# Kernel tuning notes

Hardware: AMD Instinct MI355X
Metric: run time of the kernel (lower is better)

The kernel has to match this reference:

```python
import jax, jax.numpy as jnp
import numpy as np

N = 100000       # nodes
E = 1600000      # edges (avg degree 16)
D = 128          # features_dim = hidden_dim = out_dim
G = 3            # group_num
NUM = 50000      # nodes present in all time groups
ALPHA = 0.2      # LeakyReLU slope
W_SCALE = 0.05


def setup_inputs() -> dict:
    key = jax.random.key(0)
    ks = jax.random.split(key, 8)
    x = jax.random.normal(ks[0], (N, D), jnp.float32)
    edge_index = jax.random.randint(ks[1], (2, E), 0, N, dtype=jnp.int64)
    past = jax.random.normal(ks[2], (G - 1, NUM, D), jnp.float32)
    W1 = jax.random.normal(ks[3], (2 * D, D), jnp.float32) * W_SCALE
    W2 = jax.random.normal(ks[4], (2 * D, D), jnp.float32) * W_SCALE
    W0 = jax.random.normal(ks[5], (D, D), jnp.float32) * W_SCALE
    Wp = jax.random.normal(ks[6], (G - 1, D, D), jnp.float32) * W_SCALE
    W_T = jax.random.normal(ks[7], (2 * D, D), jnp.float32) * W_SCALE
    return {"x": x, "past": past, "W1": W1, "W2": W2, "W0": W0,
            "Wp": Wp, "W_T": W_T, "edge_index": edge_index, "num": NUM}


def reference(x, past, W1, W2, W0, Wp, W_T, edge_index, num):
    src, dst = edge_index[0], edge_index[1]
    n = x.shape[0]
    deg = jax.ops.segment_sum(jnp.ones(src.shape[0], x.dtype), dst, num_segments=n)
    deg = jnp.maximum(deg, 1.0)[:, None]

    def sage_layer(h, W):
        # mean-aggregate neighbors, concat with self, linear + ReLU
        agg = jax.ops.segment_sum(h[src], dst, num_segments=n) / deg
        return jax.nn.relu(jnp.concatenate([h, agg], axis=1) @ W)

    feat = sage_layer(x, W1)      # [N, D]
    feat = sage_layer(feat, W2)   # [N, D]

    # temporal mean aggregation (dropout is identity in eval mode)
    time_feat = (feat[:num] @ W0 + jnp.einsum('knd,kde->ne', past, Wp)) / G
    fused = jnp.concatenate([feat[:num], time_feat], axis=1) @ W_T  # [num, D]
    f = jax.nn.leaky_relu(fused, ALPHA)
    f = f / jnp.maximum(jnp.linalg.norm(f, axis=1, keepdims=True), 1e-12)
    return jnp.concatenate([f, feat[num:]], axis=0)  # [N, D]
```

## Files before the change

kernel.cpp:

```cpp
#include <hip/hip_runtime.h>

#define FD 128
#define CAP 64
#define BSH 8
#define BINSZ 256
#define NBMAX 512
#define BINCAP 4864

typedef __attribute__((ext_vector_type(8))) short bf16x8;
typedef __attribute__((ext_vector_type(4))) float f32x4;

__device__ __forceinline__ float bflo(unsigned v) { return __uint_as_float(v << 16); }
__device__ __forceinline__ float bfhi(unsigned v) { return __uint_as_float(v & 0xffff0000u); }
__device__ __forceinline__ unsigned short f2b(float f) {
  unsigned u = __float_as_uint(f);
  return (unsigned short)((u + 0x7fffu + ((u >> 16) & 1u)) >> 16);
}
__device__ __forceinline__ unsigned pack2(float x, float y) {
  return (unsigned)f2b(x) | ((unsigned)f2b(y) << 16);
}

#if __has_builtin(__builtin_amdgcn_fdot2_f32_bf16)
#define HAVE_DOT2 1
typedef __attribute__((ext_vector_type(2))) __bf16 bf16x2;
__device__ __forceinline__ float dot2acc(unsigned v, unsigned w, float acc) {
  return __builtin_amdgcn_fdot2_f32_bf16(__builtin_bit_cast(bf16x2, v),
                                         __builtin_bit_cast(bf16x2, w), acc, false);
}
#endif

__device__ __forceinline__ void wpack_tile(const float* __restrict__ W,
                                           unsigned short* __restrict__ Wf,
                                           int nkt, int tt, int lane) {
  int ct = tt & 7, kt = tt >> 3;
  int m = lane & 15, q = lane >> 4;
  int nn = ct * 16 + m;
  int k0 = kt * 32 + q * 8;
  unsigned short tmp[8];
#pragma unroll
  for (int j = 0; j < 8; ++j) tmp[j] = f2b(W[(size_t)(k0 + j) * FD + nn]);
  unsigned short* dst = Wf + ((size_t)(ct * nkt + kt) * 64 + lane) * 8;
  *(uint4*)dst = *(uint4*)tmp;
}

__global__ __launch_bounds__(256) void k_prep(const float4* __restrict__ x4,
                                              unsigned short* __restrict__ xb, int total4,
                                              const float* __restrict__ W1,
                                              const float* __restrict__ W2,
                                              const float* __restrict__ W0,
                                              const float* __restrict__ Wp,
                                              const float* __restrict__ WT,
                                              unsigned short* __restrict__ w1f,
                                              unsigned short* __restrict__ w2f,
                                              unsigned short* __restrict__ wcf,
                                              unsigned short* __restrict__ wtf,
                                              unsigned short* __restrict__ f1b,
                                              int n, int XCB) {
  int b = blockIdx.x, tid = threadIdx.x;

  if (b < XCB) {
    int i = b * 256 + tid;
    if (i < total4) {
      float4 v = x4[i];
      *(uint2*)&xb[(size_t)i * 4] = make_uint2(pack2(v.x, v.y), pack2(v.z, v.w));
    }
    return;
  }
  b -= XCB;
  if (b < 72) {
    int t4 = b * 4 + (tid >> 6);
    int lane = tid & 63;
    if (t4 < 64) wpack_tile(W1, w1f, 8, t4, lane);
    else if (t4 < 128) wpack_tile(W2, w2f, 8, t4 - 64, lane);
    else if (t4 < 192) wpack_tile(WT, wtf, 8, t4 - 128, lane);
    else {
      int tt = t4 - 192;
      int ct = tt & 7, kt = tt >> 3;
      const float* src = kt < 4 ? W0 : (kt < 8 ? Wp : (Wp + FD * FD));
      int ktl = kt & 3;
      int m = lane & 15, q = lane >> 4;
      int nn = ct * 16 + m;
      int k0 = ktl * 32 + q * 8;
      unsigned short tmp[8];
#pragma unroll
      for (int j = 0; j < 8; ++j) tmp[j] = f2b(src[(size_t)(k0 + j) * FD + nn]);
      unsigned short* dstp = wcf + ((size_t)(ct * 12 + kt) * 64 + lane) * 8;
      *(uint4*)dstp = *(uint4*)tmp;
    }
    return;
  }
  if (tid < 64) ((unsigned*)&xb[(size_t)n * FD])[tid] = 0u;
  else if (tid < 128) ((unsigned*)&f1b[(size_t)n * FD])[tid - 64] = 0u;
}

__global__ __launch_bounds__(256) void k_binscatter(const int* __restrict__ src,
                                                    const int* __restrict__ dst,
                                                    int* __restrict__ binCur,
                                                    unsigned* __restrict__ binned,
                                                    int E, int n, int NB) {
  __shared__ int lcnt[NBMAX], lbase[NBMAX];
  int t = threadIdx.x;
  for (int i = t; i < NB; i += 256) lcnt[i] = 0;
  __syncthreads();

  const int CH = 4096;
  int e0 = blockIdx.x * CH;
  int se[16], de[16];
#pragma unroll
  for (int k = 0; k < 16; ++k) {
    int e = e0 + k * 256 + t;
    int ok = e < E;
    unsigned s = ok ? (unsigned)src[e] : 0u;
    unsigned d = ok ? (unsigned)dst[e] : 0u;
    if (s >= (unsigned)n) s = 0;
    ok = ok && d < (unsigned)n;
    se[k] = (int)s;
    de[k] = ok ? (int)d : -1;
    if (ok) atomicAdd(&lcnt[d >> BSH], 1);
  }
  __syncthreads();
  for (int i = t; i < NB; i += 256) {
    int c = lcnt[i];
    lbase[i] = c ? atomicAdd(&binCur[i], c) : 0;
    lcnt[i] = 0;
  }
  __syncthreads();
#pragma unroll
  for (int k = 0; k < 16; ++k) {
    if (de[k] >= 0) {
      int bb = de[k] >> BSH;
      int p = lbase[bb] + atomicAdd(&lcnt[bb], 1);
      if (p < BINCAP)
        binned[(size_t)bb * BINCAP + p] = ((unsigned)(de[k] & 255) << 24) | (unsigned)se[k];
    }
  }
}

__global__ __launch_bounds__(256) void k_bucket(const unsigned* __restrict__ binned,
                                                const int* __restrict__ binCur,
                                                int* __restrict__ cnt,
                                                int* __restrict__ idx, int n) {
  __shared__ int lcnt[BINSZ];
  int bin = blockIdx.x, t = threadIdx.x;
  int c0 = min(binCur[bin], BINCAP);
  lcnt[t] = 0;
  __syncthreads();

  int base = bin << BSH;
  const unsigned* seg = binned + (size_t)bin * BINCAP;
  for (int i = t; i < c0; i += 256) {
    unsigned pr = seg[i];
    int dlow = (int)(pr >> 24);
    int p = atomicAdd(&lcnt[dlow], 1);
    if (p < CAP) idx[(size_t)(base + dlow) * CAP + p] = (int)(pr & 0xFFFFFFu);
  }
  __syncthreads();
  int d = base + t;
  if (d < n) cnt[d] = lcnt[t];
}

template <int FUSE>
__global__ __launch_bounds__(256) void k_sage(const unsigned* __restrict__ hb,
                                              const int* __restrict__ cnt,
                                              const int* __restrict__ idx,
                                              const unsigned short* __restrict__ Wf,
                                              const float* __restrict__ past,
                                              const unsigned short* __restrict__ wcf,
                                              const unsigned short* __restrict__ wtf,
                                              float* __restrict__ outf,
                                              unsigned short* __restrict__ outb,
                                              int n, int num) {
  constexpr int SAW = FUSE ? 392 : 264;
  __shared__ unsigned short sa[32][SAW];
  int tid = threadIdx.x;
  int lane = tid & 63, wv = tid >> 6;
  int rowBase = blockIdx.x * 32;

  for (int i = tid; i < 32 * 32; i += 256) {
    int r = i >> 5, cp = i & 31;
    int gr = rowBase + r;
    uint2 v = (gr < n) ? *(const uint2*)&hb[(size_t)gr * 64 + cp * 2] : make_uint2(0u, 0u);
    *(uint2*)&sa[r][cp * 4] = v;
  }

  int rbase = wv * 8;
  const int* ip = idx + (size_t)(rowBase + rbase) * CAP;
  int vidx[8];
  int c[8];
  int maxc = 0;
#pragma unroll
  for (int j = 0; j < 8; ++j) {
    int gr = rowBase + rbase + j;
    int cj = (gr < n) ? min(cnt[gr], CAP) : 0;
    cj = __builtin_amdgcn_readfirstlane(cj);
    c[j] = cj;
    maxc = max(maxc, cj);
    int v = 0;
    if (lane < cj) v = ip[j * CAP + lane];
    vidx[j] = v;
  }
  maxc = min(maxc, CAP);

  float4 pf[FUSE ? 8 : 1];
  if (FUSE) {
    bool doPast = (rowBase < num);
    const float4* pastBase = (const float4*)past;
#pragma unroll
    for (int w = 0; w < 8; ++w) {
      int li = w * 256 + tid;
      int half = li >> 10;
      int r = (li >> 5) & 31;
      int c4 = li & 31;
      int gr = rowBase + r;
      float4 v = {0.f, 0.f, 0.f, 0.f};
      if (doPast && gr < num) v = pastBase[((size_t)half * num + gr) * 32 + c4];
      pf[w] = v;
    }
  }

#ifdef HAVE_DOT2
  float sxa[8], dxa[8];
#pragma unroll
  for (int j = 0; j < 8; ++j) { sxa[j] = 0.f; dxa[j] = 0.f; }
  const unsigned ONES = 0x3F803F80u;
  const unsigned PMON = 0xBF803F80u;

  for (int e = 0; e < maxc; e += 4) {
    int l1 = min(e + 1, CAP - 1), l2 = min(e + 2, CAP - 1), l3 = min(e + 3, CAP - 1);
    unsigned v[8][4];
#pragma unroll
    for (int j = 0; j < 8; ++j) {
      int s0 = __builtin_amdgcn_readlane(vidx[j], e);
      int s1 = __builtin_amdgcn_readlane(vidx[j], l1);
      int s2 = __builtin_amdgcn_readlane(vidx[j], l2);
      int s3 = __builtin_amdgcn_readlane(vidx[j], l3);
      s0 = (e     < c[j]) ? s0 : n;
      s1 = (e + 1 < c[j]) ? s1 : n;
      s2 = (e + 2 < c[j]) ? s2 : n;
      s3 = (e + 3 < c[j]) ? s3 : n;
      v[j][0] = hb[(size_t)s0 * 64 + lane];
      v[j][1] = hb[(size_t)s1 * 64 + lane];
      v[j][2] = hb[(size_t)s2 * 64 + lane];
      v[j][3] = hb[(size_t)s3 * 64 + lane];
    }
#pragma unroll
    for (int j = 0; j < 8; ++j) {
#pragma unroll
      for (int k = 0; k < 4; ++k) {
        sxa[j] = dot2acc(v[j][k], ONES, sxa[j]);
        dxa[j] = dot2acc(v[j][k], PMON, dxa[j]);
      }
    }
  }
#pragma unroll
  for (int j = 0; j < 8; ++j) {
    float inv = 0.5f / fmaxf((float)c[j], 1.0f);
    float ax = (sxa[j] + dxa[j]) * inv;
    float ay = (sxa[j] - dxa[j]) * inv;
    *(unsigned*)&sa[rbase + j][FD + lane * 2] = pack2(ax, ay);
  }
#else
  float ax[8], ay[8];
#pragma unroll
  for (int j = 0; j < 8; ++j) { ax[j] = 0.f; ay[j] = 0.f; }
  for (int e = 0; e < maxc; e += 4) {
    int l1 = min(e + 1, CAP - 1), l2 = min(e + 2, CAP - 1), l3 = min(e + 3, CAP - 1);
    unsigned v[8][4];
#pragma unroll
    for (int j = 0; j < 8; ++j) {
      int s0 = __builtin_amdgcn_readlane(vidx[j], e);
      int s1 = __builtin_amdgcn_readlane(vidx[j], l1);
      int s2 = __builtin_amdgcn_readlane(vidx[j], l2);
      int s3 = __builtin_amdgcn_readlane(vidx[j], l3);
      s0 = (e     < c[j]) ? s0 : n;
      s1 = (e + 1 < c[j]) ? s1 : n;
      s2 = (e + 2 < c[j]) ? s2 : n;
      s3 = (e + 3 < c[j]) ? s3 : n;
      v[j][0] = hb[(size_t)s0 * 64 + lane];
      v[j][1] = hb[(size_t)s1 * 64 + lane];
      v[j][2] = hb[(size_t)s2 * 64 + lane];
      v[j][3] = hb[(size_t)s3 * 64 + lane];
    }
#pragma unroll
    for (int j = 0; j < 8; ++j) {
#pragma unroll
      for (int k = 0; k < 4; ++k) {
        ax[j] += bflo(v[j][k]);
        ay[j] += bfhi(v[j][k]);
      }
    }
  }
#pragma unroll
  for (int j = 0; j < 8; ++j) {
    float inv = 1.0f / fmaxf((float)c[j], 1.0f);
    *(unsigned*)&sa[rbase + j][FD + lane * 2] = pack2(ax[j] * inv, ay[j] * inv);
  }
#endif
  __syncthreads();

  int m = lane & 15, q = lane >> 4;
  f32x4 z = {0.f, 0.f, 0.f, 0.f};
  f32x4 acc[2][2] = {{z, z}, {z, z}};
  int ct0 = wv * 2;
  const bf16x8* WfV = (const bf16x8*)Wf;
#pragma unroll
  for (int kt = 0; kt < 8; ++kt) {
    bf16x8 a0 = *(const bf16x8*)&sa[m][kt * 32 + q * 8];
    bf16x8 a1 = *(const bf16x8*)&sa[16 + m][kt * 32 + q * 8];
    bf16x8 b0 = WfV[(size_t)(ct0 * 8 + kt) * 64 + lane];
    bf16x8 b1 = WfV[(size_t)((ct0 + 1) * 8 + kt) * 64 + lane];
    acc[0][0] = __builtin_amdgcn_mfma_f32_16x16x32_bf16(a0, b0, acc[0][0], 0, 0, 0);
    acc[0][1] = __builtin_amdgcn_mfma_f32_16x16x32_bf16(a0, b1, acc[0][1], 0, 0, 0);
    acc[1][0] = __builtin_amdgcn_mfma_f32_16x16x32_bf16(a1, b0, acc[1][0], 0, 0, 0);
    acc[1][1] = __builtin_amdgcn_mfma_f32_16x16x32_bf16(a1, b1, acc[1][1], 0, 0, 0);
  }

  if (!FUSE) {
#pragma unroll
    for (int rt = 0; rt < 2; ++rt)
#pragma unroll
      for (int t = 0; t < 2; ++t) {
        int col = (ct0 + t) * 16 + m;
#pragma unroll
        for (int reg = 0; reg < 4; ++reg) {
          int gr = rowBase + rt * 16 + q * 4 + reg;
          if (gr < n) outb[(size_t)gr * FD + col] = f2b(fmaxf(acc[rt][t][reg], 0.f));
        }
      }
    return;
  }

  if (rowBase >= num) {
#pragma unroll
    for (int rt = 0; rt < 2; ++rt)
#pragma unroll
      for (int t = 0; t < 2; ++t) {
        int col = (ct0 + t) * 16 + m;
#pragma unroll
        for (int reg = 0; reg < 4; ++reg) {
          int gr = rowBase + rt * 16 + q * 4 + reg;
          if (gr < n) outf[(size_t)gr * FD + col] = fmaxf(acc[rt][t][reg], 0.f);
        }
      }
    return;
  }

  __syncthreads();

#pragma unroll
  for (int rt = 0; rt < 2; ++rt)
#pragma unroll
    for (int t = 0; t < 2; ++t) {
      int col = (ct0 + t) * 16 + m;
#pragma unroll
      for (int reg = 0; reg < 4; ++reg) {
        int r = rt * 16 + q * 4 + reg;
        int gr = rowBase + r;
        float v = fmaxf(acc[rt][t][reg], 0.f);
        if (gr >= num) {
          if (gr < n) outf[(size_t)gr * FD + col] = v;
          v = 0.f;
        }
        sa[r][col] = f2b(v);
      }
    }

#pragma unroll
  for (int w = 0; w < 8; ++w) {
    int li = w * 256 + tid;
    int half = li >> 10;
    int r = (li >> 5) & 31;
    int c4 = li & 31;
    *(uint2*)&sa[r][(half ? 256 : FD) + c4 * 4] =
        make_uint2(pack2(pf[w].x, pf[w].y), pack2(pf[w].z, pf[w].w));
  }
  __syncthreads();

  const bf16x8* WcV = (const bf16x8*)wcf;
  const bf16x8* WtV = (const bf16x8*)wtf;

  f32x4 accA[2][2] = {{z, z}, {z, z}};
#pragma unroll
  for (int kt = 0; kt < 12; ++kt) {
    bf16x8 a0 = *(const bf16x8*)&sa[m][kt * 32 + q * 8];
    bf16x8 a1 = *(const bf16x8*)&sa[16 + m][kt * 32 + q * 8];
    bf16x8 b0 = WcV[(size_t)(ct0 * 12 + kt) * 64 + lane];
    bf16x8 b1 = WcV[(size_t)((ct0 + 1) * 12 + kt) * 64 + lane];
    accA[0][0] = __builtin_amdgcn_mfma_f32_16x16x32_bf16(a0, b0, accA[0][0], 0, 0, 0);
    accA[0][1] = __builtin_amdgcn_mfma_f32_16x16x32_bf16(a0, b1, accA[0][1], 0, 0, 0);
    accA[1][0] = __builtin_amdgcn_mfma_f32_16x16x32_bf16(a1, b0, accA[1][0], 0, 0, 0);
    accA[1][1] = __builtin_amdgcn_mfma_f32_16x16x32_bf16(a1, b1, accA[1][1], 0, 0, 0);
  }
  __syncthreads();

  const float inv3 = 1.0f / 3.0f;
#pragma unroll
  for (int rt = 0; rt < 2; ++rt)
#pragma unroll
    for (int t = 0; t < 2; ++t) {
      int col = (ct0 + t) * 16 + m;
#pragma unroll
      for (int reg = 0; reg < 4; ++reg)
        sa[rt * 16 + q * 4 + reg][FD + col] = f2b(accA[rt][t][reg] * inv3);
    }
  __syncthreads();

  f32x4 acc2[2][2] = {{z, z}, {z, z}};
#pragma unroll
  for (int kt = 0; kt < 8; ++kt) {
    bf16x8 a0 = *(const bf16x8*)&sa[m][kt * 32 + q * 8];
    bf16x8 a1 = *(const bf16x8*)&sa[16 + m][kt * 32 + q * 8];
    bf16x8 b0 = WtV[(size_t)(ct0 * 8 + kt) * 64 + lane];
    bf16x8 b1 = WtV[(size_t)((ct0 + 1) * 8 + kt) * 64 + lane];
    acc2[0][0] = __builtin_amdgcn_mfma_f32_16x16x32_bf16(a0, b0, acc2[0][0], 0, 0, 0);
    acc2[0][1] = __builtin_amdgcn_mfma_f32_16x16x32_bf16(a0, b1, acc2[0][1], 0, 0, 0);
    acc2[1][0] = __builtin_amdgcn_mfma_f32_16x16x32_bf16(a1, b0, acc2[1][0], 0, 0, 0);
    acc2[1][1] = __builtin_amdgcn_mfma_f32_16x16x32_bf16(a1, b1, acc2[1][1], 0, 0, 0);
  }
  __syncthreads();

  float* sof = (float*)&sa[0][0];
#pragma unroll
  for (int rt = 0; rt < 2; ++rt)
#pragma unroll
    for (int t = 0; t < 2; ++t) {
      int col = (ct0 + t) * 16 + m;
#pragma unroll
      for (int reg = 0; reg < 4; ++reg) {
        float v = acc2[rt][t][reg];
        sof[(rt * 16 + q * 4 + reg) * 132 + col] = v > 0.f ? v : 0.2f * v;
      }
    }
  __syncthreads();

#pragma unroll
  for (int j = 0; j < 8; ++j) {
    int r = wv * 8 + j;
    float v0 = sof[r * 132 + lane * 2], v1 = sof[r * 132 + lane * 2 + 1];
    float ss = v0 * v0 + v1 * v1;
#pragma unroll
    for (int mk = 32; mk >= 1; mk >>= 1) ss += __shfl_xor(ss, mk, 64);
    float inv = 1.0f / fmaxf(sqrtf(ss), 1e-12f);
    int gr = rowBase + r;
    if (gr < num) {
      float2 o = {v0 * inv, v1 * inv};
      *(float2*)&outf[(size_t)gr * FD + lane * 2] = o;
    }
  }
}

extern "C" void kernel_launch(void* const* d_in, const int* in_sizes, int n_in,
                              void* d_out, int out_size, void* d_ws, size_t ws_size,
                              hipStream_t stream) {
  const float* x    = (const float*)d_in[0];
  const float* past = (const float*)d_in[1];
  const float* W1   = (const float*)d_in[2];
  const float* W2   = (const float*)d_in[3];
  const float* W0   = (const float*)d_in[4];
  const float* Wp   = (const float*)d_in[5];
  const float* WT   = (const float*)d_in[6];
  const int*   ei   = (const int*)d_in[7];

  int N   = in_sizes[0] / FD;
  int NUM = in_sizes[1] / (2 * FD);
  int E   = in_sizes[7] / 2;
  const int* src = ei;
  const int* dst = ei + E;
  float* out = (float*)d_out;

  int NB = (N + BINSZ - 1) >> BSH;

  char* p = (char*)d_ws;
  int* cnt      = (int*)p;  p += (((size_t)N * 4 + 255) & ~(size_t)255);
  int* idx      = (int*)p;  p += (size_t)N * CAP * 4;
  int* binCur   = (int*)p;  p += NBMAX * 4;
  unsigned* binned = (unsigned*)p; p += (size_t)NB * BINCAP * 4;
  unsigned short* xb  = (unsigned short*)p; p += (size_t)(N + 1) * FD * 2;
  unsigned short* f1b = (unsigned short*)p; p += (size_t)(N + 1) * FD * 2;
  unsigned short* w1f = (unsigned short*)p; p += (size_t)8 * 8 * 64 * 8 * 2;
  unsigned short* w2f = (unsigned short*)p; p += (size_t)8 * 8 * 64 * 8 * 2;
  unsigned short* wcf = (unsigned short*)p; p += (size_t)8 * 12 * 64 * 8 * 2;
  unsigned short* wtf = (unsigned short*)p;

  hipMemsetAsync(binCur, 0, NBMAX * sizeof(int), stream);

  k_binscatter<<<(E + 4095) / 4096, 256, 0, stream>>>(src, dst, binCur, binned, E, N, NB);

  int total4 = N * 32;
  int XCB = (total4 + 255) / 256;
  k_prep<<<XCB + 72 + 1, 256, 0, stream>>>((const float4*)x, xb, total4,
                                           W1, W2, W0, Wp, WT,
                                           w1f, w2f, wcf, wtf, f1b, N, XCB);

  k_bucket<<<NB, 256, 0, stream>>>(binned, binCur, cnt, idx, N);

  int sageGrid = (N + 31) / 32;
  k_sage<0><<<sageGrid, 256, 0, stream>>>((const unsigned*)xb, cnt, idx, w1f,
                                          nullptr, nullptr, nullptr,
                                          nullptr, f1b, N, N);
  k_sage<1><<<sageGrid, 256, 0, stream>>>((const unsigned*)f1b, cnt, idx, w2f,
                                          past, wcf, wtf,
                                          out, nullptr, N, NUM);
}
```

Baseline: 354.7 us.

## Fuse edge bin-scatter into prep kernel with larger chunks and wider conversion

Merges the edge bin-scatter pass into the prep kernel so one launch covers edge binning, x-to-bf16 conversion and weight packing. The scatter blocks now handle 16384 edges each and re-read src/dst in a second pass instead of holding them in registers. The x conversion handles two float4s per thread. This saves a launch and lets the binning overlap with the conversion work, at the cost of reloading edges and running fewer, longer scatter blocks with fewer global atomics.

```diff
diff --git a/kernel.cpp b/kernel.cpp
--- a/kernel.cpp
+++ b/kernel.cpp
@@ -6,6 +6,7 @@
 #define BINSZ 256
 #define NBMAX 512
 #define BINCAP 4864
+#define SCH 16384
 
 typedef __attribute__((ext_vector_type(8))) short bf16x8;
 typedef __attribute__((ext_vector_type(4))) float f32x4;
@@ -43,7 +44,12 @@
   *(uint4*)dst = *(uint4*)tmp;
 }
 
-__global__ __launch_bounds__(256) void k_prep(const float4* __restrict__ x4,
+__global__ __launch_bounds__(256) void k_prep(const int* __restrict__ src,
+                                              const int* __restrict__ dst,
+                                              int* __restrict__ binCur,
+                                              unsigned* __restrict__ binned,
+                                              int E, int NB,
+                                              const float4* __restrict__ x4,
                                               unsigned short* __restrict__ xb, int total4,
                                               const float* __restrict__ W1,
                                               const float* __restrict__ W2,
@@ -55,85 +61,80 @@
                                               unsigned short* __restrict__ wcf,
                                               unsigned short* __restrict__ wtf,
                                               unsigned short* __restrict__ f1b,
-                                              int n, int XCB) {
-  int b = blockIdx.x, tid = threadIdx.x;
-
+                                              int n, int SCB, int XCB) {
+  __shared__ int lcnt[NBMAX], lbase[NBMAX];
+  int b = blockIdx.x, t = threadIdx.x;
+
+  if (b < SCB) {
+    for (int i = t; i < NB; i += 256) lcnt[i] = 0;
+    __syncthreads();
+    int e0 = b * SCH;
+#pragma unroll 4
+    for (int k = 0; k < SCH / 256; ++k) {
+      int e = e0 + k * 256 + t;
+      if (e < E) {
+        unsigned d = (unsigned)dst[e];
+        if (d < (unsigned)n) atomicAdd(&lcnt[d >> BSH], 1);
+      }
+    }
+    __syncthreads();
+    for (int i = t; i < NB; i += 256) {
+      int c = lcnt[i];
+      lbase[i] = c ? atomicAdd(&binCur[i], c) : 0;
+      lcnt[i] = 0;
+    }
+    __syncthreads();
+#pragma unroll 4
+    for (int k = 0; k < SCH / 256; ++k) {
+      int e = e0 + k * 256 + t;
+      if (e < E) {
+        unsigned s = (unsigned)src[e], d = (unsigned)dst[e];
+        if (s >= (unsigned)n) s = 0;
+        if (d < (unsigned)n) {
+          int bb = (int)(d >> BSH);
+          int p = lbase[bb] + atomicAdd(&lcnt[bb], 1);
+          if (p < BINCAP)
+            binned[(size_t)bb * BINCAP + p] = ((d & 255u) << 24) | s;
+        }
+      }
+    }
+    return;
+  }
+  b -= SCB;
   if (b < XCB) {
-    int i = b * 256 + tid;
-    if (i < total4) {
-      float4 v = x4[i];
-      *(uint2*)&xb[(size_t)i * 4] = make_uint2(pack2(v.x, v.y), pack2(v.z, v.w));
+    int i = b * 256 + t;
+    if (i * 2 < total4) {
+      float4 v0 = x4[i * 2], v1 = x4[i * 2 + 1];
+      *(uint4*)&xb[(size_t)i * 8] = make_uint4(pack2(v0.x, v0.y), pack2(v0.z, v0.w),
+                                               pack2(v1.x, v1.y), pack2(v1.z, v1.w));
     }
     return;
   }
   b -= XCB;
   if (b < 72) {
-    int t4 = b * 4 + (tid >> 6);
-    int lane = tid & 63;
+    int t4 = b * 4 + (t >> 6);
+    int lane = t & 63;
     if (t4 < 64) wpack_tile(W1, w1f, 8, t4, lane);
     else if (t4 < 128) wpack_tile(W2, w2f, 8, t4 - 64, lane);
     else if (t4 < 192) wpack_tile(WT, wtf, 8, t4 - 128, lane);
     else {
       int tt = t4 - 192;
       int ct = tt & 7, kt = tt >> 3;
-      const float* src = kt < 4 ? W0 : (kt < 8 ? Wp : (Wp + FD * FD));
+      const float* srcp = kt < 4 ? W0 : (kt < 8 ? Wp : (Wp + FD * FD));
       int ktl = kt & 3;
       int m = lane & 15, q = lane >> 4;
       int nn = ct * 16 + m;
       int k0 = ktl * 32 + q * 8;
       unsigned short tmp[8];
 #pragma unroll
-      for (int j = 0; j < 8; ++j) tmp[j] = f2b(src[(size_t)(k0 + j) * FD + nn]);
+      for (int j = 0; j < 8; ++j) tmp[j] = f2b(srcp[(size_t)(k0 + j) * FD + nn]);
       unsigned short* dstp = wcf + ((size_t)(ct * 12 + kt) * 64 + lane) * 8;
       *(uint4*)dstp = *(uint4*)tmp;
     }
     return;
   }
-  if (tid < 64) ((unsigned*)&xb[(size_t)n * FD])[tid] = 0u;
-  else if (tid < 128) ((unsigned*)&f1b[(size_t)n * FD])[tid - 64] = 0u;
-}
-
-__global__ __launch_bounds__(256) void k_binscatter(const int* __restrict__ src,
-                                                    const int* __restrict__ dst,
-                                                    int* __restrict__ binCur,
-                                                    unsigned* __restrict__ binned,
-                                                    int E, int n, int NB) {
-  __shared__ int lcnt[NBMAX], lbase[NBMAX];
-  int t = threadIdx.x;
-  for (int i = t; i < NB; i += 256) lcnt[i] = 0;
-  __syncthreads();
-
-  const int CH = 4096;
-  int e0 = blockIdx.x * CH;
-  int se[16], de[16];
-#pragma unroll
-  for (int k = 0; k < 16; ++k) {
-    int e = e0 + k * 256 + t;
-    int ok = e < E;
-    unsigned s = ok ? (unsigned)src[e] : 0u;
-    unsigned d = ok ? (unsigned)dst[e] : 0u;
-    if (s >= (unsigned)n) s = 0;
-    ok = ok && d < (unsigned)n;
-    se[k] = (int)s;
-    de[k] = ok ? (int)d : -1;
-    if (ok) atomicAdd(&lcnt[d >> BSH], 1);
-  }
-  __syncthreads();
-  for (int i = t; i < NB; i += 256) {
-    int c = lcnt[i];
-    lbase[i] = c ? atomicAdd(&binCur[i], c) : 0;
-    lcnt[i] = 0;
-  }
-  __syncthreads();
-#pragma unroll
-  for (int k = 0; k < 16; ++k) {
-    if (de[k] >= 0) {
-      int bb = de[k] >> BSH;
-      int p = lbase[bb] + atomicAdd(&lcnt[bb], 1);
-      if (p < BINCAP)
-        binned[(size_t)bb * BINCAP + p] = ((unsigned)(de[k] & 255) << 24) | (unsigned)se[k];
-    }
-  }
+  if (t < 64) ((unsigned*)&xb[(size_t)n * FD])[t] = 0u;
+  else if (t < 128) ((unsigned*)&f1b[(size_t)n * FD])[t - 64] = 0u;
 }
 
 __global__ __launch_bounds__(256) void k_bucket(const unsigned* __restrict__ binned,
@@ -484,13 +485,13 @@
 
   hipMemsetAsync(binCur, 0, NBMAX * sizeof(int), stream);
 
-  k_binscatter<<<(E + 4095) / 4096, 256, 0, stream>>>(src, dst, binCur, binned, E, N, NB);
-
   int total4 = N * 32;
-  int XCB = (total4 + 255) / 256;
-  k_prep<<<XCB + 72 + 1, 256, 0, stream>>>((const float4*)x, xb, total4,
-                                           W1, W2, W0, Wp, WT,
-                                           w1f, w2f, wcf, wtf, f1b, N, XCB);
+  int SCB = (E + SCH - 1) / SCH;
+  int XCB = (total4 / 2 + 255) / 256;
+  k_prep<<<SCB + XCB + 72 + 1, 256, 0, stream>>>(src, dst, binCur, binned, E, NB,
+                                                 (const float4*)x, xb, total4,
+                                                 W1, W2, W0, Wp, WT,
+                                                 w1f, w2f, wcf, wtf, f1b, N, SCB, XCB);
 
   k_bucket<<<NB, 256, 0, stream>>>(binned, binCur, cnt, idx, N);
 
```

New measurement: 398.9 us. +12.5%, slower.
